# Optimization experiments

Measured on AMD Instinct MI355X. Metric: run time of the kernel, lower is better.

## Reference

```python
import jax, jax.numpy as jnp
import numpy as np

N, IN_DIM, HID = 8192, 128, 64
LEAKY_SLOPE = 0.2
MASK_VAL = -9e15


def lstm_step(x, W_ih, W_hh, b_ih, b_hh, h0, c0):
    # PyTorch LSTM single time step, gate order i, f, g, o
    gates = x @ W_ih.T + b_ih + h0 @ W_hh.T + b_hh
    i, f, g, o = jnp.split(gates, 4, axis=-1)
    c = jax.nn.sigmoid(f) * c0 + jax.nn.sigmoid(i) * jnp.tanh(g)
    h = jax.nn.sigmoid(o) * jnp.tanh(c)
    return h, c


def setup_inputs() -> dict:
    key = jax.random.key(0)
    ks = jax.random.split(key, 10)
    sc = 0.05
    x = jax.random.normal(ks[0], (N, IN_DIM), jnp.float32)
    adj = jax.random.randint(ks[1], (N, N), 0, 2).astype(jnp.float32)
    fea_W = jax.random.normal(ks[2], (IN_DIM, HID), jnp.float32) * sc
    fea_b = jnp.zeros((HID,), jnp.float32)
    gat_W = jax.random.normal(ks[3], (HID, IN_DIM), jnp.float32) * sc
    gat_a = jax.random.normal(ks[4], (2 * IN_DIM,), jnp.float32) * sc
    enc_W_ih = jax.random.normal(ks[5], (4 * HID, IN_DIM), jnp.float32) * sc
    enc_W_hh = jax.random.normal(ks[6], (4 * HID, HID), jnp.float32) * sc
    enc_b_ih = jnp.zeros((4 * HID,), jnp.float32)
    enc_b_hh = jnp.zeros((4 * HID,), jnp.float32)
    dec_W_ih = jax.random.normal(ks[7], (4 * IN_DIM, HID), jnp.float32) * sc
    dec_W_hh = jax.random.normal(ks[8], (4 * IN_DIM, IN_DIM), jnp.float32) * sc
    dec_b_ih = jnp.zeros((4 * IN_DIM,), jnp.float32)
    dec_b_hh = jnp.zeros((4 * IN_DIM,), jnp.float32)
    return dict(x=x, adj=adj, fea_W=fea_W, fea_b=fea_b, gat_W=gat_W, gat_a=gat_a,
                enc_W_ih=enc_W_ih, enc_W_hh=enc_W_hh, enc_b_ih=enc_b_ih, enc_b_hh=enc_b_hh,
                dec_W_ih=dec_W_ih, dec_W_hh=dec_W_hh, dec_b_ih=dec_b_ih, dec_b_hh=dec_b_hh)


def reference(x, adj, fea_W, fea_b, gat_W, gat_a,
              enc_W_ih, enc_W_hh, enc_b_ih, enc_b_hh,
              dec_W_ih, dec_W_hh, dec_b_ih, dec_b_hh):
    # structure branch: Linear + ReLU then GAT layer
    structure = jax.nn.relu(x @ fea_W + fea_b)            # [N, HID]
    Wh = structure @ gat_W                                # [N, IN_DIM]
    a1, a2 = gat_a[:IN_DIM], gat_a[IN_DIM:]
    e = jax.nn.leaky_relu((Wh @ a1)[:, None] + (Wh @ a2)[None, :], LEAKY_SLOPE)  # [N, N]
    scores = jnp.where(adj > 0, e, MASK_VAL)
    att = jax.nn.softmax(scores, axis=1)
    emb = jax.nn.elu(att @ Wh)                            # [N, IN_DIM]
    # attribute branch: seq_len=1 encoder/decoder LSTM with zero init states
    h0e = jnp.zeros((N, HID), x.dtype)
    h_enc, _ = lstm_step(x, enc_W_ih, enc_W_hh, enc_b_ih, enc_b_hh, h0e, h0e)
    h0d = jnp.zeros((N, IN_DIM), x.dtype)
    att_adj, _ = lstm_step(h_enc, dec_W_ih, dec_W_hh, dec_b_ih, dec_b_hh, h0d, h0d)  # [N, IN_DIM]
    con_adj = emb @ emb.T                                 # [N, N]
    return con_adj, att_adj
```

## Files before the change

kernel.cpp:

```cpp
#include <hip/hip_runtime.h>
#include <hip/hip_bf16.h>

typedef __hip_bfloat16 bf16_t;
typedef short bf16x8 __attribute__((ext_vector_type(8)));
typedef float f32x4 __attribute__((ext_vector_type(4)));

#define NROW 8192
#define LEAKY 0.2f

__device__ __forceinline__ float b2f(bf16_t v){ return __bfloat162float(v); }
__device__ __forceinline__ unsigned short f2b(float f){
  union { bf16_t h; unsigned short u; } cv; cv.h = __float2bfloat16(f); return cv.u;
}
__device__ __forceinline__ float sigf(float v){ return 1.0f / (1.0f + __expf(-v)); }

__global__ void k_probe(const unsigned short* __restrict__ x_raw, int* __restrict__ flag)
{
  const int lane = threadIdx.x;
  int cnt = 0;
  for (int k = lane; k < 512; k += 64){
    const int e = (x_raw[k] >> 7) & 0xff;
    cnt += (e >= 120 && e <= 130) ? 1 : 0;
  }
  #pragma unroll
  for (int s = 1; s < 64; s <<= 1) cnt += __shfl_xor(cnt, s, 64);
  if (lane == 0) flag[0] = (cnt < 384) ? 1 : 0;
}

__global__ __launch_bounds__(256) void k_cvt(
    const void* __restrict__ encW, const void* __restrict__ decW,
    const int* __restrict__ flag,
    unsigned short* __restrict__ encWb, unsigned short* __restrict__ decWb)
{
  const int idx = blockIdx.x*256 + threadIdx.x;
  const int isf32 = flag[0];
  if (idx < 32768){
    float v = isf32 ? ((const float*)encW)[idx] : b2f(((const bf16_t*)encW)[idx]);
    encWb[idx] = f2b(v);
  } else {
    const int j = idx - 32768;
    float v = isf32 ? ((const float*)decW)[j] : b2f(((const bf16_t*)decW)[j]);
    decWb[j] = f2b(v);
  }
}

__global__ __launch_bounds__(256) void k_feamask(
    const void* __restrict__ x, const void* __restrict__ adj,
    const void* __restrict__ fea_W, const void* __restrict__ fea_b,
    const void* __restrict__ gat_W, const void* __restrict__ gat_a,
    const int* __restrict__ flag,
    unsigned short* __restrict__ Whb_p, float* __restrict__ s1, float* __restrict__ s2,
    unsigned short* __restrict__ xb, unsigned char* __restrict__ mask8)
{
  const int r = blockIdx.x, tid = threadIdx.x;
  const int isf32 = flag[0];

  float4 mv0, mv1, mv2, mv3, mv4, mv5, mv6, mv7;
  bf16x8 bv0, bv1, bv2, bv3;
  if (isf32){
    const float4* arow = (const float4*)((const float*)adj + (size_t)r*NROW);
    mv0 = arow[(size_t)tid*2];         mv1 = arow[(size_t)tid*2+1];
    mv2 = arow[(size_t)(tid+256)*2];   mv3 = arow[(size_t)(tid+256)*2+1];
    mv4 = arow[(size_t)(tid+512)*2];   mv5 = arow[(size_t)(tid+512)*2+1];
    mv6 = arow[(size_t)(tid+768)*2];   mv7 = arow[(size_t)(tid+768)*2+1];
  } else {
    const unsigned short* arow = (const unsigned short*)adj + (size_t)r*NROW;
    bv0 = *(const bf16x8*)(arow + (size_t)tid*8);
    bv1 = *(const bf16x8*)(arow + (size_t)(tid+256)*8);
    bv2 = *(const bf16x8*)(arow + (size_t)(tid+512)*8);
    bv3 = *(const bf16x8*)(arow + (size_t)(tid+768)*8);
  }

  if (tid < 64){
    const int l = tid;
    float x0, x1;
    if (isf32){
      const float* xr = (const float*)x + (size_t)r*128;
      x0 = xr[l]; x1 = xr[l+64];
    } else {
      const bf16_t* xr = (const bf16_t*)x + (size_t)r*128;
      x0 = b2f(xr[l]); x1 = b2f(xr[l+64]);
    }
    xb[(size_t)r*128 + l]      = f2b(x0);
    xb[(size_t)r*128 + 64 + l] = f2b(x1);

    float acc = isf32 ? ((const float*)fea_b)[l] : b2f(((const bf16_t*)fea_b)[l]);
    if (isf32){
      const float* W = (const float*)fea_W;
      #pragma unroll
      for (int d=0; d<64; ++d) acc = fmaf(__shfl(x0, d, 64), W[d*64+l], acc);
      #pragma unroll
      for (int d=0; d<64; ++d) acc = fmaf(__shfl(x1, d, 64), W[(d+64)*64+l], acc);
    } else {
      const bf16_t* W = (const bf16_t*)fea_W;
      #pragma unroll
      for (int d=0; d<64; ++d) acc = fmaf(__shfl(x0, d, 64), b2f(W[d*64+l]), acc);
      #pragma unroll
      for (int d=0; d<64; ++d) acc = fmaf(__shfl(x1, d, 64), b2f(W[(d+64)*64+l]), acc);
    }
    const float stv = fmaxf(acc, 0.0f);

    float w0 = 0.f, w1 = 0.f;
    if (isf32){
      const float* W = (const float*)gat_W;
      #pragma unroll
      for (int d=0; d<64; ++d){
        const float sd = __shfl(stv, d, 64);
        w0 = fmaf(sd, W[d*128+l],    w0);
        w1 = fmaf(sd, W[d*128+64+l], w1);
      }
    } else {
      const bf16_t* W = (const bf16_t*)gat_W;
      #pragma unroll
      for (int d=0; d<64; ++d){
        const float sd = __shfl(stv, d, 64);
        w0 = fmaf(sd, b2f(W[d*128+l]),    w0);
        w1 = fmaf(sd, b2f(W[d*128+64+l]), w1);
      }
    }

    const size_t pbase = (size_t)(r >> 3)*1024 + (r & 7);
    Whb_p[pbase + (size_t)l*8]      = f2b(w0);
    Whb_p[pbase + (size_t)(l+64)*8] = f2b(w1);

    float a10, a11, a20, a21;
    if (isf32){
      const float* A = (const float*)gat_a;
      a10 = A[l]; a11 = A[l+64]; a20 = A[128+l]; a21 = A[192+l];
    } else {
      const bf16_t* A = (const bf16_t*)gat_a;
      a10 = b2f(A[l]); a11 = b2f(A[l+64]); a20 = b2f(A[128+l]); a21 = b2f(A[192+l]);
    }
    float r1 = w0*a10 + w1*a11;
    float r2 = w0*a20 + w1*a21;
    #pragma unroll
    for (int s=1; s<64; s<<=1){ r1 += __shfl_xor(r1, s, 64); r2 += __shfl_xor(r2, s, 64); }
    if (l == 0){ s1[r] = r1; s2[r] = r2; }
  }

  if (isf32){
    const float4 va[8] = { mv0, mv1, mv2, mv3, mv4, mv5, mv6, mv7 };
    #pragma unroll
    for (int k=0;k<4;++k){
      const float4 v0 = va[2*k], v1 = va[2*k+1];
      unsigned int m =
          (unsigned int)(v0.x>0.f)      | ((unsigned int)(v0.y>0.f)<<1) |
          ((unsigned int)(v0.z>0.f)<<2) | ((unsigned int)(v0.w>0.f)<<3) |
          ((unsigned int)(v1.x>0.f)<<4) | ((unsigned int)(v1.y>0.f)<<5) |
          ((unsigned int)(v1.z>0.f)<<6) | ((unsigned int)(v1.w>0.f)<<7);
      mask8[(size_t)r*1024 + tid + k*256] = (unsigned char)m;
    }
  } else {
    const bf16x8 vb[4] = { bv0, bv1, bv2, bv3 };
    #pragma unroll
    for (int k=0;k<4;++k){
      unsigned int m = 0;
      #pragma unroll
      for (int j=0;j<8;++j){
        union { short s; unsigned short u; } cv; cv.s = vb[k][j];
        union { unsigned short u; bf16_t h; } cv2; cv2.u = cv.u;
        m |= ((unsigned int)(b2f(cv2.h) > 0.f)) << j;
      }
      mask8[(size_t)r*1024 + tid + k*256] = (unsigned char)m;
    }
  }
}

__global__ __launch_bounds__(256) void k_enc2(
    const unsigned short* __restrict__ xb, const unsigned short* __restrict__ Wb,
    const void* __restrict__ b_ih, const void* __restrict__ b_hh,
    const int* __restrict__ flag, unsigned short* __restrict__ h_enc_b)
{
  __shared__ float g_lds[32][257];
  const int tid = threadIdx.x, lane = tid & 63, wv = tid >> 6;
  const int quad = lane >> 4, nn = lane & 15;
  const int rowbase = blockIdx.x * 32;
  const int rows_off = (wv & 1) * 16;
  const int col_off  = (wv >> 1) * 128;

  f32x4 acc[8];
  #pragma unroll
  for (int t=0;t<8;++t) acc[t] = (f32x4){0.f,0.f,0.f,0.f};

  #pragma unroll
  for (int ks=0; ks<4; ++ks){
    const int kb = ks*32 + quad*8;
    bf16x8 afrag = *(const bf16x8*)(xb + (size_t)(rowbase + rows_off + nn)*128 + kb);
    #pragma unroll
    for (int t=0;t<8;++t){
      bf16x8 bfrag = *(const bf16x8*)(Wb + (size_t)(col_off + t*16 + nn)*128 + kb);
      acc[t] = __builtin_amdgcn_mfma_f32_16x16x32_bf16(afrag, bfrag, acc[t], 0, 0, 0);
    }
  }
  #pragma unroll
  for (int t=0;t<8;++t)
    #pragma unroll
    for (int r=0;r<4;++r)
      g_lds[rows_off + quad*4 + r][col_off + t*16 + nn] = acc[t][r];
  __syncthreads();

  const int isf32 = flag[0];
  #pragma unroll
  for (int k=0;k<8;++k){
    const int idx = tid + k*256;
    const int r = idx >> 6, hid = idx & 63;
    float bi, bg, bo;
    if (isf32){
      const float* bi1 = (const float*)b_ih; const float* bi2 = (const float*)b_hh;
      bi = bi1[hid]     + bi2[hid];
      bg = bi1[128+hid] + bi2[128+hid];
      bo = bi1[192+hid] + bi2[192+hid];
    } else {
      const bf16_t* bi1 = (const bf16_t*)b_ih; const bf16_t* bi2 = (const bf16_t*)b_hh;
      bi = b2f(bi1[hid])     + b2f(bi2[hid]);
      bg = b2f(bi1[128+hid]) + b2f(bi2[128+hid]);
      bo = b2f(bi1[192+hid]) + b2f(bi2[192+hid]);
    }
    const float gi = g_lds[r][hid]     + bi;
    const float gg = g_lds[r][128+hid] + bg;
    const float go = g_lds[r][192+hid] + bo;
    const float c = tanhf(gg) * sigf(gi);
    const float h = tanhf(c)  * sigf(go);
    h_enc_b[(size_t)(rowbase + r)*64 + hid] = f2b(h);
  }
}

__global__ __launch_bounds__(256) void k_dec2(
    const unsigned short* __restrict__ hb, const unsigned short* __restrict__ Wb,
    const void* __restrict__ b_ih, const void* __restrict__ b_hh,
    const int* __restrict__ flag, void* __restrict__ d_out)
{
  __shared__ float g_lds[16][517];
  const int tid = threadIdx.x, lane = tid & 63, wv = tid >> 6;
  const int quad = lane >> 4, nn = lane & 15;
  const int rowbase = blockIdx.x * 16;
  const int col_off = wv * 128;

  f32x4 acc[8];
  #pragma unroll
  for (int t=0;t<8;++t) acc[t] = (f32x4){0.f,0.f,0.f,0.f};

  #pragma unroll
  for (int ks=0; ks<2; ++ks){
    const int kb = ks*32 + quad*8;
    bf16x8 afrag = *(const bf16x8*)(hb + (size_t)(rowbase + nn)*64 + kb);
    #pragma unroll
    for (int t=0;t<8;++t){
      bf16x8 bfrag = *(const bf16x8*)(Wb + (size_t)(col_off + t*16 + nn)*64 + kb);
      acc[t] = __builtin_amdgcn_mfma_f32_16x16x32_bf16(afrag, bfrag, acc[t], 0, 0, 0);
    }
  }
  #pragma unroll
  for (int t=0;t<8;++t)
    #pragma unroll
    for (int r=0;r<4;++r)
      g_lds[quad*4 + r][col_off + t*16 + nn] = acc[t][r];
  __syncthreads();

  const int isf32 = flag[0];
  #pragma unroll
  for (int k=0;k<8;++k){
    const int idx = tid + k*256;
    const int r = idx >> 7, col = idx & 127;
    float bi, bg, bo;
    if (isf32){
      const float* b1 = (const float*)b_ih; const float* b2 = (const float*)b_hh;
      bi = b1[col]     + b2[col];
      bg = b1[256+col] + b2[256+col];
      bo = b1[384+col] + b2[384+col];
    } else {
      const bf16_t* b1 = (const bf16_t*)b_ih; const bf16_t* b2v = (const bf16_t*)b_hh;
      bi = b2f(b1[col])     + b2f(b2v[col]);
      bg = b2f(b1[256+col]) + b2f(b2v[256+col]);
      bo = b2f(b1[384+col]) + b2f(b2v[384+col]);
    }
    const float gi = g_lds[r][col]     + bi;
    const float gg = g_lds[r][256+col] + bg;
    const float go = g_lds[r][384+col] + bo;
    const float c = tanhf(gg) * sigf(gi);
    const float h = tanhf(c)  * sigf(go);
    const size_t oidx = (size_t)NROW*NROW + (size_t)(rowbase + r)*128 + col;
    if (isf32) ((float*)d_out)[oidx] = h;
    else       ((unsigned short*)d_out)[oidx] = f2b(h);
  }
}

__global__ __launch_bounds__(512) void k_attn32(
    const unsigned char* __restrict__ mask8, const unsigned short* __restrict__ Whb_p,
    const float* __restrict__ s1g, const float* __restrict__ s2g,
    unsigned short* __restrict__ emb_p)
{
  __shared__ float C_lds[8][16*128];
  __shared__ float dn_lds[8][32];
  const int tid  = threadIdx.x;
  const int lane = tid & 63;
  const int wv   = tid >> 6;
  const int quad = lane >> 4;
  const int mrow = lane & 15;
  const int rowbase = blockIdx.x * 32;
  const float s1r0 = s1g[rowbase + mrow];
  const float s1r1 = s1g[rowbase + 16 + mrow];
  const unsigned char* mp0 = mask8 + (size_t)(rowbase + mrow) * 1024;
  const unsigned char* mp1 = mask8 + (size_t)(rowbase + 16 + mrow) * 1024;

  f32x4 acc[2][8];
  #pragma unroll
  for (int g=0;g<2;++g)
    #pragma unroll
    for (int t=0;t<8;++t) acc[g][t] = (f32x4){0.f,0.f,0.f,0.f};
  float dn0 = 0.f, dn1 = 0.f;

  const int jbeg = wv * 1024;
  for (int j0 = jbeg; j0 < jbeg + 1024; j0 += 128){
    uint4 mw0 = *(const uint4*)(mp0 + (j0 >> 3));
    uint4 mw1 = *(const uint4*)(mp1 + (j0 >> 3));
    #pragma unroll
    for (int t4=0; t4<4; ++t4){
      const unsigned int mb0 = ((((const unsigned int*)&mw0)[t4]) >> (8*quad)) & 0xffu;
      const unsigned int mb1 = ((((const unsigned int*)&mw1)[t4]) >> (8*quad)) & 0xffu;
      const int kb = j0 + t4*32 + quad*8;
      float4 s2a = *(const float4*)(s2g + kb);
      float4 s2b = *(const float4*)(s2g + kb + 4);
      const float sv[8] = { s2a.x, s2a.y, s2a.z, s2a.w, s2b.x, s2b.y, s2b.z, s2b.w };
      bf16x8 af0, af1;
      #pragma unroll
      for (int b=0;b<8;++b){
        float v0 = s1r0 + sv[b];
        v0 = (v0 > 0.f) ? v0 : LEAKY * v0;
        const float e0 = __expf(v0);
        const float p0 = (mb0 & (1u<<b)) ? e0 : 0.f;
        dn0 += p0;
        af0[b] = (short)f2b(p0);
        float v1 = s1r1 + sv[b];
        v1 = (v1 > 0.f) ? v1 : LEAKY * v1;
        const float e1 = __expf(v1);
        const float p1 = (mb1 & (1u<<b)) ? e1 : 0.f;
        dn1 += p1;
        af1[b] = (short)f2b(p1);
      }
      const unsigned short* wb = Whb_p + (size_t)(kb >> 3)*1024 + mrow*8;
      #pragma unroll
      for (int t=0;t<8;++t){
        bf16x8 bfrag = *(const bf16x8*)(wb + t*128);
        acc[0][t] = __builtin_amdgcn_mfma_f32_16x16x32_bf16(af0, bfrag, acc[0][t], 0, 0, 0);
        acc[1][t] = __builtin_amdgcn_mfma_f32_16x16x32_bf16(af1, bfrag, acc[1][t], 0, 0, 0);
      }
    }
  }

  dn0 += __shfl_xor(dn0, 16, 64);
  dn0 += __shfl_xor(dn0, 32, 64);
  dn1 += __shfl_xor(dn1, 16, 64);
  dn1 += __shfl_xor(dn1, 32, 64);
  if (lane < 16){ dn_lds[wv][lane] = dn0; dn_lds[wv][16 + lane] = dn1; }

  #pragma unroll
  for (int rg=0; rg<2; ++rg){
    #pragma unroll
    for (int t=0;t<8;++t){
      #pragma unroll
      for (int r=0;r<4;++r)
        C_lds[wv][(quad*4+r)*128 + t*16 + mrow] = acc[rg][t][r];
    }
    __syncthreads();
    for (int idx = tid; idx < 16*128; idx += 512){
      const int m = idx >> 7;
      const int d = idx & 127;
      float v = C_lds[0][idx] + C_lds[1][idx] + C_lds[2][idx] + C_lds[3][idx]
              + C_lds[4][idx] + C_lds[5][idx] + C_lds[6][idx] + C_lds[7][idx];
      const float den = dn_lds[0][rg*16+m] + dn_lds[1][rg*16+m] + dn_lds[2][rg*16+m]
                      + dn_lds[3][rg*16+m] + dn_lds[4][rg*16+m] + dn_lds[5][rg*16+m]
                      + dn_lds[6][rg*16+m] + dn_lds[7][rg*16+m];
      v /= den;
      v = (v > 0.f) ? v : (__expf(v) - 1.f);
      emb_p[(size_t)(d >> 3)*65536 + (size_t)(rowbase + rg*16 + m)*8 + (d & 7)] = f2b(v);
    }
    __syncthreads();
  }
}

__global__ __launch_bounds__(256) void k_out(
    const unsigned short* __restrict__ emb_p, const int* __restrict__ flag,
    void* __restrict__ d_out)
{
  const int tid  = threadIdx.x;
  const int lane = tid & 63, wv = tid >> 6;
  const int quad = lane >> 4, nn = lane & 15;
  const int i0 = blockIdx.y * 128 + wv * 32;
  const int j0 = blockIdx.x * 64;

  f32x4 acc[2][4];
  #pragma unroll
  for (int a=0;a<2;++a)
    #pragma unroll
    for (int b=0;b<4;++b) acc[a][b] = (f32x4){0.f,0.f,0.f,0.f};

  #pragma unroll
  for (int ks=0; ks<4; ++ks){
    const int kb = ks*32 + quad*8;
    const unsigned short* base = emb_p + (size_t)(kb >> 3)*65536;
    bf16x8 a0 = *(const bf16x8*)(base + (size_t)(i0 + nn)*8);
    bf16x8 a1 = *(const bf16x8*)(base + (size_t)(i0 + 16 + nn)*8);
    #pragma unroll
    for (int t=0;t<4;++t){
      bf16x8 b = *(const bf16x8*)(base + (size_t)(j0 + t*16 + nn)*8);
      acc[0][t] = __builtin_amdgcn_mfma_f32_16x16x32_bf16(a0, b, acc[0][t], 0, 0, 0);
      acc[1][t] = __builtin_amdgcn_mfma_f32_16x16x32_bf16(a1, b, acc[1][t], 0, 0, 0);
    }
  }

  const int isf32 = flag[0];
  if (isf32){
    float* out = (float*)d_out;
    #pragma unroll
    for (int mi=0; mi<2; ++mi)
      #pragma unroll
      for (int t=0;t<4;++t)
        #pragma unroll
        for (int r=0;r<4;++r)
          out[(size_t)(i0 + mi*16 + quad*4 + r)*NROW + j0 + t*16 + nn] = acc[mi][t][r];
  } else {
    unsigned short* out = (unsigned short*)d_out;
    #pragma unroll
    for (int mi=0; mi<2; ++mi)
      #pragma unroll
      for (int t=0;t<4;++t)
        #pragma unroll
        for (int r=0;r<4;++r)
          out[(size_t)(i0 + mi*16 + quad*4 + r)*NROW + j0 + t*16 + nn] = f2b(acc[mi][t][r]);
  }
}

extern "C" void kernel_launch(void* const* d_in, const int* in_sizes, int n_in,
                              void* d_out, int out_size, void* d_ws, size_t ws_size,
                              hipStream_t stream)
{
  (void)in_sizes; (void)n_in; (void)out_size; (void)ws_size;
  const void* x        = d_in[0];
  const void* adj      = d_in[1];
  const void* fea_W    = d_in[2];
  const void* fea_b    = d_in[3];
  const void* gat_W    = d_in[4];
  const void* gat_a    = d_in[5];
  const void* enc_W_ih = d_in[6];
  const void* enc_b_ih = d_in[8];
  const void* enc_b_hh = d_in[9];
  const void* dec_W_ih = d_in[10];
  const void* dec_b_ih = d_in[12];
  const void* dec_b_hh = d_in[13];

  char* ws = (char*)d_ws;
  unsigned short* Whb_p   = (unsigned short*)ws;
  unsigned short* emb_p   = (unsigned short*)(ws + (2u<<20));
  unsigned short* xb      = (unsigned short*)(ws + (4u<<20));
  unsigned short* h_enc_b = (unsigned short*)(ws + (6u<<20));
  unsigned char*  mask8   = (unsigned char*) (ws + (7u<<20));
  float* s1    = (float*)(ws + (15u<<20));
  float* s2    = (float*)(ws + (15u<<20) + 32768);
  unsigned short* encWb = (unsigned short*)(ws + (15u<<20) + 65536);
  unsigned short* decWb = (unsigned short*)(ws + (15u<<20) + 65536 + 65536);
  int* flag = (int*)(ws + (15u<<20) + 3*65536);

  k_probe<<<1, 64, 0, stream>>>((const unsigned short*)x, flag);
  k_cvt<<<256, 256, 0, stream>>>(enc_W_ih, dec_W_ih, flag, encWb, decWb);
  k_feamask<<<NROW, 256, 0, stream>>>(x, adj, fea_W, fea_b, gat_W, gat_a, flag,
                                      Whb_p, s1, s2, xb, mask8);
  k_enc2<<<256, 256, 0, stream>>>(xb, encWb, enc_b_ih, enc_b_hh, flag, h_enc_b);
  k_dec2<<<512, 256, 0, stream>>>(h_enc_b, decWb, dec_b_ih, dec_b_hh, flag, d_out);
  k_attn32<<<256, 512, 0, stream>>>(mask8, Whb_p, s1, s2, emb_p);
  k_out<<<dim3(128, 64), 256, 0, stream>>>(emb_p, flag, d_out);
}
```

Measured before the change: 571.9 us.

## Read adjacency directly in attention kernel instead of precomputing bitmask

Removes the separate adjacency-to-bitmask pass and its 8 MB mask buffer. The attention kernel now reads the raw adjacency rows (fp32 or bf16) and tests each entry itself, while the feature kernel shrinks to one 64-thread wave per row. This drops one full write and re-read of a mask. In exchange the attention kernel reads 256 MB of fp32 adjacency in its inner loop with scattered per-lane 32-byte loads, which may stall the MFMA pipeline.

Result: slower. 588.8 us (+3.0%).

```diff
diff --git a/kernel.cpp b/kernel.cpp
--- a/kernel.cpp
+++ b/kernel.cpp
@@ -44,126 +44,80 @@
   }
 }
 
-__global__ __launch_bounds__(256) void k_feamask(
-    const void* __restrict__ x, const void* __restrict__ adj,
+__global__ __launch_bounds__(64) void k_fea(
+    const void* __restrict__ x,
     const void* __restrict__ fea_W, const void* __restrict__ fea_b,
     const void* __restrict__ gat_W, const void* __restrict__ gat_a,
     const int* __restrict__ flag,
     unsigned short* __restrict__ Whb_p, float* __restrict__ s1, float* __restrict__ s2,
-    unsigned short* __restrict__ xb, unsigned char* __restrict__ mask8)
-{
-  const int r = blockIdx.x, tid = threadIdx.x;
-  const int isf32 = flag[0];
-
-  float4 mv0, mv1, mv2, mv3, mv4, mv5, mv6, mv7;
-  bf16x8 bv0, bv1, bv2, bv3;
-  if (isf32){
-    const float4* arow = (const float4*)((const float*)adj + (size_t)r*NROW);
-    mv0 = arow[(size_t)tid*2];         mv1 = arow[(size_t)tid*2+1];
-    mv2 = arow[(size_t)(tid+256)*2];   mv3 = arow[(size_t)(tid+256)*2+1];
-    mv4 = arow[(size_t)(tid+512)*2];   mv5 = arow[(size_t)(tid+512)*2+1];
-    mv6 = arow[(size_t)(tid+768)*2];   mv7 = arow[(size_t)(tid+768)*2+1];
-  } else {
-    const unsigned short* arow = (const unsigned short*)adj + (size_t)r*NROW;
-    bv0 = *(const bf16x8*)(arow + (size_t)tid*8);
-    bv1 = *(const bf16x8*)(arow + (size_t)(tid+256)*8);
-    bv2 = *(const bf16x8*)(arow + (size_t)(tid+512)*8);
-    bv3 = *(const bf16x8*)(arow + (size_t)(tid+768)*8);
-  }
-
-  if (tid < 64){
-    const int l = tid;
-    float x0, x1;
-    if (isf32){
-      const float* xr = (const float*)x + (size_t)r*128;
-      x0 = xr[l]; x1 = xr[l+64];
-    } else {
-      const bf16_t* xr = (const bf16_t*)x + (size_t)r*128;
-      x0 = b2f(xr[l]); x1 = b2f(xr[l+64]);
-    }
-    xb[(size_t)r*128 + l]      = f2b(x0);
-    xb[(size_t)r*128 + 64 + l] = f2b(x1);
-
-    float acc = isf32 ? ((const float*)fea_b)[l] : b2f(((const bf16_t*)fea_b)[l]);
-    if (isf32){
-      const float* W = (const float*)fea_W;
-      #pragma unroll
-      for (int d=0; d<64; ++d) acc = fmaf(__shfl(x0, d, 64), W[d*64+l], acc);
-      #pragma unroll
-      for (int d=0; d<64; ++d) acc = fmaf(__shfl(x1, d, 64), W[(d+64)*64+l], acc);
-    } else {
-      const bf16_t* W = (const bf16_t*)fea_W;
-      #pragma unroll
-      for (int d=0; d<64; ++d) acc = fmaf(__shfl(x0, d, 64), b2f(W[d*64+l]), acc);
-      #pragma unroll
-      for (int d=0; d<64; ++d) acc = fmaf(__shfl(x1, d, 64), b2f(W[(d+64)*64+l]), acc);
-    }
-    const float stv = fmaxf(acc, 0.0f);
-
-    float w0 = 0.f, w1 = 0.f;
-    if (isf32){
-      const float* W = (const float*)gat_W;
-      #pragma unroll
-      for (int d=0; d<64; ++d){
-        const float sd = __shfl(stv, d, 64);
-        w0 = fmaf(sd, W[d*128+l],    w0);
-        w1 = fmaf(sd, W[d*128+64+l], w1);
-      }
-    } else {
-      const bf16_t* W = (const bf16_t*)gat_W;
-      #pragma unroll
-      for (int d=0; d<64; ++d){
-        const float sd = __shfl(stv, d, 64);
-        w0 = fmaf(sd, b2f(W[d*128+l]),    w0);
-        w1 = fmaf(sd, b2f(W[d*128+64+l]), w1);
-      }
-    }
-
-    const size_t pbase = (size_t)(r >> 3)*1024 + (r & 7);
-    Whb_p[pbase + (size_t)l*8]      = f2b(w0);
-    Whb_p[pbase + (size_t)(l+64)*8] = f2b(w1);
-
-    float a10, a11, a20, a21;
-    if (isf32){
-      const float* A = (const float*)gat_a;
-      a10 = A[l]; a11 = A[l+64]; a20 = A[128+l]; a21 = A[192+l];
-    } else {
-      const bf16_t* A = (const bf16_t*)gat_a;
-      a10 = b2f(A[l]); a11 = b2f(A[l+64]); a20 = b2f(A[128+l]); a21 = b2f(A[192+l]);
-    }
-    float r1 = w0*a10 + w1*a11;
-    float r2 = w0*a20 + w1*a21;
-    #pragma unroll
-    for (int s=1; s<64; s<<=1){ r1 += __shfl_xor(r1, s, 64); r2 += __shfl_xor(r2, s, 64); }
-    if (l == 0){ s1[r] = r1; s2[r] = r2; }
-  }
-
-  if (isf32){
-    const float4 va[8] = { mv0, mv1, mv2, mv3, mv4, mv5, mv6, mv7 };
-    #pragma unroll
-    for (int k=0;k<4;++k){
-      const float4 v0 = va[2*k], v1 = va[2*k+1];
-      unsigned int m =
-          (unsigned int)(v0.x>0.f)      | ((unsigned int)(v0.y>0.f)<<1) |
-          ((unsigned int)(v0.z>0.f)<<2) | ((unsigned int)(v0.w>0.f)<<3) |
-          ((unsigned int)(v1.x>0.f)<<4) | ((unsigned int)(v1.y>0.f)<<5) |
-          ((unsigned int)(v1.z>0.f)<<6) | ((unsigned int)(v1.w>0.f)<<7);
-      mask8[(size_t)r*1024 + tid + k*256] = (unsigned char)m;
-    }
-  } else {
-    const bf16x8 vb[4] = { bv0, bv1, bv2, bv3 };
-    #pragma unroll
-    for (int k=0;k<4;++k){
-      unsigned int m = 0;
-      #pragma unroll
-      for (int j=0;j<8;++j){
-        union { short s; unsigned short u; } cv; cv.s = vb[k][j];
-        union { unsigned short u; bf16_t h; } cv2; cv2.u = cv.u;
-        m |= ((unsigned int)(b2f(cv2.h) > 0.f)) << j;
-      }
-      mask8[(size_t)r*1024 + tid + k*256] = (unsigned char)m;
-    }
-  }
+    unsigned short* __restrict__ xb)
+{
+  const int r = blockIdx.x, l = threadIdx.x;
+  const int isf32 = flag[0];
+
+  float x0, x1;
+  if (isf32){
+    const float* xr = (const float*)x + (size_t)r*128;
+    x0 = xr[l]; x1 = xr[l+64];
+  } else {
+    const bf16_t* xr = (const bf16_t*)x + (size_t)r*128;
+    x0 = b2f(xr[l]); x1 = b2f(xr[l+64]);
+  }
+  xb[(size_t)r*128 + l]      = f2b(x0);
+  xb[(size_t)r*128 + 64 + l] = f2b(x1);
+
+  float acc = isf32 ? ((const float*)fea_b)[l] : b2f(((const bf16_t*)fea_b)[l]);
+  if (isf32){
+    const float* W = (const float*)fea_W;
+    #pragma unroll
+    for (int d=0; d<64; ++d) acc = fmaf(__shfl(x0, d, 64), W[d*64+l], acc);
+    #pragma unroll
+    for (int d=0; d<64; ++d) acc = fmaf(__shfl(x1, d, 64), W[(d+64)*64+l], acc);
+  } else {
+    const bf16_t* W = (const bf16_t*)fea_W;
+    #pragma unroll
+    for (int d=0; d<64; ++d) acc = fmaf(__shfl(x0, d, 64), b2f(W[d*64+l]), acc);
+    #pragma unroll
+    for (int d=0; d<64; ++d) acc = fmaf(__shfl(x1, d, 64), b2f(W[(d+64)*64+l]), acc);
+  }
+  const float stv = fmaxf(acc, 0.0f);
+
+  float w0 = 0.f, w1 = 0.f;
+  if (isf32){
+    const float* W = (const float*)gat_W;
+    #pragma unroll
+    for (int d=0; d<64; ++d){
+      const float sd = __shfl(stv, d, 64);
+      w0 = fmaf(sd, W[d*128+l],    w0);
+      w1 = fmaf(sd, W[d*128+64+l], w1);
+    }
+  } else {
+    const bf16_t* W = (const bf16_t*)gat_W;
+    #pragma unroll
+    for (int d=0; d<64; ++d){
+      const float sd = __shfl(stv, d, 64);
+      w0 = fmaf(sd, b2f(W[d*128+l]),    w0);
+      w1 = fmaf(sd, b2f(W[d*128+64+l]), w1);
+    }
+  }
+
+  const size_t pbase = (size_t)(r >> 3)*1024 + (r & 7);
+  Whb_p[pbase + (size_t)l*8]      = f2b(w0);
+  Whb_p[pbase + (size_t)(l+64)*8] = f2b(w1);
+
+  float a10, a11, a20, a21;
+  if (isf32){
+    const float* A = (const float*)gat_a;
+    a10 = A[l]; a11 = A[l+64]; a20 = A[128+l]; a21 = A[192+l];
+  } else {
+    const bf16_t* A = (const bf16_t*)gat_a;
+    a10 = b2f(A[l]); a11 = b2f(A[l+64]); a20 = b2f(A[128+l]); a21 = b2f(A[192+l]);
+  }
+  float r1 = w0*a10 + w1*a11;
+  float r2 = w0*a20 + w1*a21;
+  #pragma unroll
+  for (int s=1; s<64; s<<=1){ r1 += __shfl_xor(r1, s, 64); r2 += __shfl_xor(r2, s, 64); }
+  if (l == 0){ s1[r] = r1; s2[r] = r2; }
 }
 
 __global__ __launch_bounds__(256) void k_enc2(
@@ -286,7 +240,8 @@
 }
 
 __global__ __launch_bounds__(512) void k_attn32(
-    const unsigned char* __restrict__ mask8, const unsigned short* __restrict__ Whb_p,
+    const void* __restrict__ adj, const int* __restrict__ flag,
+    const unsigned short* __restrict__ Whb_p,
     const float* __restrict__ s1g, const float* __restrict__ s2g,
     unsigned short* __restrict__ emb_p)
 {
@@ -300,8 +255,7 @@
   const int rowbase = blockIdx.x * 32;
   const float s1r0 = s1g[rowbase + mrow];
   const float s1r1 = s1g[rowbase + 16 + mrow];
-  const unsigned char* mp0 = mask8 + (size_t)(rowbase + mrow) * 1024;
-  const unsigned char* mp1 = mask8 + (size_t)(rowbase + 16 + mrow) * 1024;
+  const int isf32 = flag[0];
 
   f32x4 acc[2][8];
   #pragma unroll
@@ -311,39 +265,81 @@
   float dn0 = 0.f, dn1 = 0.f;
 
   const int jbeg = wv * 1024;
-  for (int j0 = jbeg; j0 < jbeg + 1024; j0 += 128){
-    uint4 mw0 = *(const uint4*)(mp0 + (j0 >> 3));
-    uint4 mw1 = *(const uint4*)(mp1 + (j0 >> 3));
-    #pragma unroll
-    for (int t4=0; t4<4; ++t4){
-      const unsigned int mb0 = ((((const unsigned int*)&mw0)[t4]) >> (8*quad)) & 0xffu;
-      const unsigned int mb1 = ((((const unsigned int*)&mw1)[t4]) >> (8*quad)) & 0xffu;
-      const int kb = j0 + t4*32 + quad*8;
-      float4 s2a = *(const float4*)(s2g + kb);
-      float4 s2b = *(const float4*)(s2g + kb + 4);
-      const float sv[8] = { s2a.x, s2a.y, s2a.z, s2a.w, s2b.x, s2b.y, s2b.z, s2b.w };
-      bf16x8 af0, af1;
+
+  if (isf32){
+    const float* A0 = (const float*)adj + (size_t)(rowbase + mrow)*NROW;
+    const float* A1 = (const float*)adj + (size_t)(rowbase + 16 + mrow)*NROW;
+    for (int j0 = jbeg; j0 < jbeg + 1024; j0 += 128){
       #pragma unroll
-      for (int b=0;b<8;++b){
-        float v0 = s1r0 + sv[b];
-        v0 = (v0 > 0.f) ? v0 : LEAKY * v0;
-        const float e0 = __expf(v0);
-        const float p0 = (mb0 & (1u<<b)) ? e0 : 0.f;
-        dn0 += p0;
-        af0[b] = (short)f2b(p0);
-        float v1 = s1r1 + sv[b];
-        v1 = (v1 > 0.f) ? v1 : LEAKY * v1;
-        const float e1 = __expf(v1);
-        const float p1 = (mb1 & (1u<<b)) ? e1 : 0.f;
-        dn1 += p1;
-        af1[b] = (short)f2b(p1);
+      for (int t4=0; t4<4; ++t4){
+        const int kb = j0 + t4*32 + quad*8;
+        const float4 q00 = *(const float4*)(A0 + kb);
+        const float4 q01 = *(const float4*)(A0 + kb + 4);
+        const float4 q10 = *(const float4*)(A1 + kb);
+        const float4 q11 = *(const float4*)(A1 + kb + 4);
+        const float av0[8] = { q00.x,q00.y,q00.z,q00.w, q01.x,q01.y,q01.z,q01.w };
+        const float av1[8] = { q10.x,q10.y,q10.z,q10.w, q11.x,q11.y,q11.z,q11.w };
+        float4 s2a = *(const float4*)(s2g + kb);
+        float4 s2b = *(const float4*)(s2g + kb + 4);
+        const float sv[8] = { s2a.x, s2a.y, s2a.z, s2a.w, s2b.x, s2b.y, s2b.z, s2b.w };
+        bf16x8 af0, af1;
+        #pragma unroll
+        for (int b=0;b<8;++b){
+          float v0 = s1r0 + sv[b];
+          v0 = (v0 > 0.f) ? v0 : LEAKY * v0;
+          const float p0 = (av0[b] > 0.f) ? __expf(v0) : 0.f;
+          dn0 += p0;
+          af0[b] = (short)f2b(p0);
+          float v1 = s1r1 + sv[b];
+          v1 = (v1 > 0.f) ? v1 : LEAKY * v1;
+          const float p1 = (av1[b] > 0.f) ? __expf(v1) : 0.f;
+          dn1 += p1;
+          af1[b] = (short)f2b(p1);
+        }
+        const unsigned short* wb = Whb_p + (size_t)(kb >> 3)*1024 + mrow*8;
+        #pragma unroll
+        for (int t=0;t<8;++t){
+          bf16x8 bfrag = *(const bf16x8*)(wb + t*128);
+          acc[0][t] = __builtin_amdgcn_mfma_f32_16x16x32_bf16(af0, bfrag, acc[0][t], 0, 0, 0);
+          acc[1][t] = __builtin_amdgcn_mfma_f32_16x16x32_bf16(af1, bfrag, acc[1][t], 0, 0, 0);
+        }
       }
-      const unsigned short* wb = Whb_p + (size_t)(kb >> 3)*1024 + mrow*8;
+    }
+  } else {
+    const unsigned short* A0 = (const unsigned short*)adj + (size_t)(rowbase + mrow)*NROW;
+    const unsigned short* A1 = (const unsigned short*)adj + (size_t)(rowbase + 16 + mrow)*NROW;
+    for (int j0 = jbeg; j0 < jbeg + 1024; j0 += 128){
       #pragma unroll
-      for (int t=0;t<8;++t){
-        bf16x8 bfrag = *(const bf16x8*)(wb + t*128);
-        acc[0][t] = __builtin_amdgcn_mfma_f32_16x16x32_bf16(af0, bfrag, acc[0][t], 0, 0, 0);
-        acc[1][t] = __builtin_amdgcn_mfma_f32_16x16x32_bf16(af1, bfrag, acc[1][t], 0, 0, 0);
+      for (int t4=0; t4<4; ++t4){
+        const int kb = j0 + t4*32 + quad*8;
+        const bf16x8 q0 = *(const bf16x8*)(A0 + kb);
+        const bf16x8 q1 = *(const bf16x8*)(A1 + kb);
+        float4 s2a = *(const float4*)(s2g + kb);
+        float4 s2b = *(const float4*)(s2g + kb + 4);
+        const float sv[8] = { s2a.x, s2a.y, s2a.z, s2a.w, s2b.x, s2b.y, s2b.z, s2b.w };
+        bf16x8 af0, af1;
+        #pragma unroll
+        for (int b=0;b<8;++b){
+          union { short s; unsigned short u; } c0; c0.s = q0[b];
+          union { short s; unsigned short u; } c1; c1.s = q1[b];
+          float v0 = s1r0 + sv[b];
+          v0 = (v0 > 0.f) ? v0 : LEAKY * v0;
+          const float p0 = (c0.u > 0 && c0.u < 0x8000) ? __expf(v0) : 0.f;
+          dn0 += p0;
+          af0[b] = (short)f2b(p0);
+          float v1 = s1r1 + sv[b];
+          v1 = (v1 > 0.f) ? v1 : LEAKY * v1;
+          const float p1 = (c1.u > 0 && c1.u < 0x8000) ? __expf(v1) : 0.f;
+          dn1 += p1;
+          af1[b] = (short)f2b(p1);
+        }
+        const unsigned short* wb = Whb_p + (size_t)(kb >> 3)*1024 + mrow*8;
+        #pragma unroll
+        for (int t=0;t<8;++t){
+          bf16x8 bfrag = *(const bf16x8*)(wb + t*128);
+          acc[0][t] = __builtin_amdgcn_mfma_f32_16x16x32_bf16(af0, bfrag, acc[0][t], 0, 0, 0);
+          acc[1][t] = __builtin_amdgcn_mfma_f32_16x16x32_bf16(af1, bfrag, acc[1][t], 0, 0, 0);
+        }
       }
     }
   }
@@ -454,7 +450,6 @@
   unsigned short* emb_p   = (unsigned short*)(ws + (2u<<20));
   unsigned short* xb      = (unsigned short*)(ws + (4u<<20));
   unsigned short* h_enc_b = (unsigned short*)(ws + (6u<<20));
-  unsigned char*  mask8   = (unsigned char*) (ws + (7u<<20));
   float* s1    = (float*)(ws + (15u<<20));
   float* s2    = (float*)(ws + (15u<<20) + 32768);
   unsigned short* encWb = (unsigned short*)(ws + (15u<<20) + 65536);
@@ -463,10 +458,10 @@
 
   k_probe<<<1, 64, 0, stream>>>((const unsigned short*)x, flag);
   k_cvt<<<256, 256, 0, stream>>>(enc_W_ih, dec_W_ih, flag, encWb, decWb);
-  k_feamask<<<NROW, 256, 0, stream>>>(x, adj, fea_W, fea_b, gat_W, gat_a, flag,
-                                      Whb_p, s1, s2, xb, mask8);
+  k_fea<<<NROW, 64, 0, stream>>>(x, fea_W, fea_b, gat_W, gat_a, flag,
+                                 Whb_p, s1, s2, xb);
   k_enc2<<<256, 256, 0, stream>>>(xb, encWb, enc_b_ih, enc_b_hh, flag, h_enc_b);
   k_dec2<<<512, 256, 0, stream>>>(h_enc_b, decWb, dec_b_ih, dec_b_hh, flag, d_out);
-  k_attn32<<<256, 512, 0, stream>>>(mask8, Whb_p, s1, s2, emb_p);
+  k_attn32<<<256, 512, 0, stream>>>(adj, flag, Whb_p, s1, s2, emb_p);
   k_out<<<dim3(128, 64), 256, 0, stream>>>(emb_p, flag, d_out);
 }
```

## Split attention aggregation over two key halves with a separate merge kernel

Applied to the files above, without the earlier changes.

The attention-weighted aggregation kernel now splits the key dimension into two halves, launching 512 blocks instead of 256. Each block writes fp32 partial sums and denominators to workspace. A new merge kernel adds the halves, normalises, applies ELU and writes the packed bf16 embedding. This targets poor occupancy on a GPU with many compute units, at the cost of extra global traffic for the partials and one more launch.

After: 569.6 us. Within noise of the previous version (-0.4%).

```diff
diff --git a/kernel.cpp b/kernel.cpp
--- a/kernel.cpp
+++ b/kernel.cpp
@@ -285,10 +285,10 @@
   }
 }
 
-__global__ __launch_bounds__(512) void k_attn32(
+__global__ __launch_bounds__(512) void k_attn32s(
     const unsigned char* __restrict__ mask8, const unsigned short* __restrict__ Whb_p,
     const float* __restrict__ s1g, const float* __restrict__ s2g,
-    unsigned short* __restrict__ emb_p)
+    float* __restrict__ Cpart, float* __restrict__ dnpart)
 {
   __shared__ float C_lds[8][16*128];
   __shared__ float dn_lds[8][32];
@@ -297,7 +297,9 @@
   const int wv   = tid >> 6;
   const int quad = lane >> 4;
   const int mrow = lane & 15;
-  const int rowbase = blockIdx.x * 32;
+  const int rowtile = blockIdx.x & 255;
+  const int half    = blockIdx.x >> 8;
+  const int rowbase = rowtile * 32;
   const float s1r0 = s1g[rowbase + mrow];
   const float s1r1 = s1g[rowbase + 16 + mrow];
   const unsigned char* mp0 = mask8 + (size_t)(rowbase + mrow) * 1024;
@@ -310,8 +312,8 @@
     for (int t=0;t<8;++t) acc[g][t] = (f32x4){0.f,0.f,0.f,0.f};
   float dn0 = 0.f, dn1 = 0.f;
 
-  const int jbeg = wv * 1024;
-  for (int j0 = jbeg; j0 < jbeg + 1024; j0 += 128){
+  const int jbeg = half*4096 + wv*512;
+  for (int j0 = jbeg; j0 < jbeg + 512; j0 += 128){
     uint4 mw0 = *(const uint4*)(mp0 + (j0 >> 3));
     uint4 mw1 = *(const uint4*)(mp1 + (j0 >> 3));
     #pragma unroll
@@ -354,6 +356,7 @@
   dn1 += __shfl_xor(dn1, 32, 64);
   if (lane < 16){ dn_lds[wv][lane] = dn0; dn_lds[wv][16 + lane] = dn1; }
 
+  float* Ch = Cpart + (size_t)half * NROW * 128;
   #pragma unroll
   for (int rg=0; rg<2; ++rg){
     #pragma unroll
@@ -366,16 +369,38 @@
     for (int idx = tid; idx < 16*128; idx += 512){
       const int m = idx >> 7;
       const int d = idx & 127;
-      float v = C_lds[0][idx] + C_lds[1][idx] + C_lds[2][idx] + C_lds[3][idx]
-              + C_lds[4][idx] + C_lds[5][idx] + C_lds[6][idx] + C_lds[7][idx];
-      const float den = dn_lds[0][rg*16+m] + dn_lds[1][rg*16+m] + dn_lds[2][rg*16+m]
-                      + dn_lds[3][rg*16+m] + dn_lds[4][rg*16+m] + dn_lds[5][rg*16+m]
-                      + dn_lds[6][rg*16+m] + dn_lds[7][rg*16+m];
-      v /= den;
-      v = (v > 0.f) ? v : (__expf(v) - 1.f);
-      emb_p[(size_t)(d >> 3)*65536 + (size_t)(rowbase + rg*16 + m)*8 + (d & 7)] = f2b(v);
+      const float v = C_lds[0][idx] + C_lds[1][idx] + C_lds[2][idx] + C_lds[3][idx]
+                    + C_lds[4][idx] + C_lds[5][idx] + C_lds[6][idx] + C_lds[7][idx];
+      Ch[(size_t)(rowbase + rg*16 + m)*128 + d] = v;
+      if (d == 0){
+        const float den = dn_lds[0][rg*16+m] + dn_lds[1][rg*16+m] + dn_lds[2][rg*16+m]
+                        + dn_lds[3][rg*16+m] + dn_lds[4][rg*16+m] + dn_lds[5][rg*16+m]
+                        + dn_lds[6][rg*16+m] + dn_lds[7][rg*16+m];
+        dnpart[half*NROW + rowbase + rg*16 + m] = den;
+      }
     }
     __syncthreads();
+  }
+}
+
+__global__ __launch_bounds__(256) void k_merge(
+    const float* __restrict__ Cpart, const float* __restrict__ dnpart,
+    unsigned short* __restrict__ emb_p)
+{
+  const int tid = threadIdx.x;
+  const int rowbase = blockIdx.x * 16;
+  const float* C0 = Cpart;
+  const float* C1 = Cpart + (size_t)NROW * 128;
+  #pragma unroll
+  for (int k=0;k<8;++k){
+    const int idx = tid + k*256;
+    const int m = idx >> 7;
+    const int d = idx & 127;
+    const int row = rowbase + m;
+    const float den = dnpart[row] + dnpart[NROW + row];
+    float v = (C0[(size_t)row*128 + d] + C1[(size_t)row*128 + d]) / den;
+    v = (v > 0.f) ? v : (__expf(v) - 1.f);
+    emb_p[(size_t)(d >> 3)*65536 + (size_t)row*8 + (d & 7)] = f2b(v);
   }
 }
 
@@ -460,6 +485,8 @@
   unsigned short* encWb = (unsigned short*)(ws + (15u<<20) + 65536);
   unsigned short* decWb = (unsigned short*)(ws + (15u<<20) + 65536 + 65536);
   int* flag = (int*)(ws + (15u<<20) + 3*65536);
+  float* Cpart  = (float*)(ws + (16u<<20));
+  float* dnpart = (float*)(ws + (24u<<20));
 
   k_probe<<<1, 64, 0, stream>>>((const unsigned short*)x, flag);
   k_cvt<<<256, 256, 0, stream>>>(enc_W_ih, dec_W_ih, flag, encWb, decWb);
@@ -467,6 +494,7 @@
                                       Whb_p, s1, s2, xb, mask8);
   k_enc2<<<256, 256, 0, stream>>>(xb, encWb, enc_b_ih, enc_b_hh, flag, h_enc_b);
   k_dec2<<<512, 256, 0, stream>>>(h_enc_b, decWb, dec_b_ih, dec_b_hh, flag, d_out);
-  k_attn32<<<256, 512, 0, stream>>>(mask8, Whb_p, s1, s2, emb_p);
+  k_attn32s<<<512, 512, 0, stream>>>(mask8, Whb_p, s1, s2, Cpart, dnpart);
+  k_merge<<<512, 256, 0, stream>>>(Cpart, dnpart, emb_p);
   k_out<<<dim3(128, 64), 256, 0, stream>>>(emb_p, flag, d_out);
 }
```
